# Kernel optimization log

Hardware: AMD Instinct MI355X
Metric: run time of the kernel (lower is better)

Reference implementation:

```python
import jax, jax.numpy as jnp
import numpy as np

NB_CLASSES = 10
NB_NEIGHBORS = 75  # 1 closest + 74 precomputed geodesic neighbors


def setup_inputs() -> dict:
    key = jax.random.key(0)
    k0, k1, k2, k3, k4, k5 = jax.random.split(key, 6)
    nb_data, nb_train, d = 1024, 100000, 256
    x = jax.random.normal(k0, (nb_data, d), dtype=jnp.float32)
    X = jax.random.normal(k1, (nb_train, d), dtype=jnp.float32)
    # train table is stored normalized + centered (init_nn_querier)
    X = X / jnp.linalg.norm(X, axis=1, keepdims=True)
    X = X - jnp.mean(X, axis=0)
    center = jax.random.normal(k2, (d,), dtype=jnp.float32) * 0.01
    train_labels = jax.random.randint(k3, (nb_train,), 0, NB_CLASSES).astype(jnp.int32)
    train_neighbor_index = jax.random.randint(
        k4, (nb_train, NB_NEIGHBORS - 1), 0, nb_train).astype(jnp.int32)
    cali_nonconformity = jnp.sort(
        jax.random.randint(k5, (1000,), 0, NB_NEIGHBORS)).astype(jnp.int32)
    return {
        "x": x, "X": X, "center": center,
        "train_labels": train_labels,
        "train_neighbor_index": train_neighbor_index,
        "cali_nonconformity": cali_nonconformity,
    }


def reference(x, X, center, train_labels, train_neighbor_index, cali_nonconformity):
    # --- find_train_knns: normalize query, center, closest-neighbor search ---
    xq = x / jnp.linalg.norm(x, axis=1, keepdims=True) - center  # [B, d]
    # squared euclidean distances to every train point: [B, nb_train]
    d2 = (jnp.sum(xq * xq, axis=1, keepdims=True)
          - 2.0 * (xq @ X.T)
          + jnp.sum(X * X, axis=1)[None, :])
    closest = jnp.argmin(d2, axis=1)                               # [B]
    # neighbor list = closest point prepended to its precomputed table row
    neigh = jnp.concatenate(
        [closest[:, None], train_neighbor_index[closest]], axis=1)  # [B, K]
    knns_labels = train_labels[neigh]                              # [B, K]
    # --- nonconformity: per-class bincount, #knns NOT in class ---
    counts = jnp.sum(jax.nn.one_hot(knns_labels, NB_CLASSES, dtype=jnp.int32),
                     axis=1)                                       # [B, C]
    knns_not_in_class = jnp.sum(counts, axis=1, keepdims=True) - counts
    # --- preds_conf_cred: conformal p-values via bisect_left ---
    nb_cali = cali_nonconformity.shape[0]
    pos = jnp.searchsorted(cali_nonconformity, knns_not_in_class, side='left')
    p_value = (nb_cali - pos).astype(jnp.float32) / float(nb_cali)  # [B, C]
    preds = jnp.argmax(p_value, axis=1)                             # [B]
    top2, _ = jax.lax.top_k(p_value, 2)                             # [B, 2]
    nb_data = p_value.shape[0]
    creds = jnp.zeros_like(p_value).at[jnp.arange(nb_data), preds].set(top2[:, 0])
    return creds
```

## Files before the change

### kernel.cpp

```cpp
#include <hip/hip_runtime.h>
#include <stdint.h>


typedef __attribute__((ext_vector_type(8))) short short8;
typedef __attribute__((ext_vector_type(4))) float float4v;

static __device__ __forceinline__ unsigned short bf16_rn(float f) {
    unsigned int u = __float_as_uint(f);
    unsigned int r = (u + 0x7FFFu + ((u >> 16) & 1u)) >> 16;
    return (unsigned short)r;
}

static __device__ __forceinline__ void gload_lds16(const void* g, void* l) {
    __builtin_amdgcn_global_load_lds(
        (const __attribute__((address_space(1))) unsigned int*)g,
        (__attribute__((address_space(3))) unsigned int*)l, 16, 0, 0);
}

__global__ __launch_bounds__(256) void prep_all(
    const float* __restrict__ X, const float* __restrict__ x,
    const float* __restrict__ center,
    unsigned short* __restrict__ Bh, float* __restrict__ xn2,
    unsigned short* __restrict__ Ah, float* __restrict__ xqf,
    float* __restrict__ q2a, float* __restrict__ al2q,
    unsigned int* __restrict__ scal,
    int nb_train, int Np, int B, int Mp, int train_rb)
{
    const int tid = threadIdx.x;
    __shared__ float smax[16];
    __shared__ float p1[4], p2[4], p3[4];

    if ((int)blockIdx.x < train_rb) {
        const int r   = blockIdx.x * 16 + (tid >> 4);
        const int seg = tid & 15;
        if (r >= nb_train) {
            ushort4 z = make_ushort4(0, 0, 0, 0);
            ushort4* bp = (ushort4*)(Bh + (size_t)r * 256 + seg * 16);
            bp[0] = z; bp[1] = z; bp[2] = z; bp[3] = z;
            if (seg == 0) { xn2[r] = 3.0e38f; smax[tid >> 4] = 0.f; }
        } else {
            const float* xr = X + (size_t)r * 256 + seg * 16;
            float4 v0 = ((const float4*)xr)[0];
            float4 v1 = ((const float4*)xr)[1];
            float4 v2 = ((const float4*)xr)[2];
            float4 v3 = ((const float4*)xr)[3];
            ushort4 h0, h1, h2, h3;
            h0.x = bf16_rn(v0.x); h0.y = bf16_rn(v0.y); h0.z = bf16_rn(v0.z); h0.w = bf16_rn(v0.w);
            h1.x = bf16_rn(v1.x); h1.y = bf16_rn(v1.y); h1.z = bf16_rn(v1.z); h1.w = bf16_rn(v1.w);
            h2.x = bf16_rn(v2.x); h2.y = bf16_rn(v2.y); h2.z = bf16_rn(v2.z); h2.w = bf16_rn(v2.w);
            h3.x = bf16_rn(v3.x); h3.y = bf16_rn(v3.y); h3.z = bf16_rn(v3.z); h3.w = bf16_rn(v3.w);
            ushort4* bp = (ushort4*)(Bh + (size_t)r * 256 + seg * 16);
            bp[0] = h0; bp[1] = h1; bp[2] = h2; bp[3] = h3;
            float ss = v0.x * v0.x + v0.y * v0.y + v0.z * v0.z + v0.w * v0.w
                     + v1.x * v1.x + v1.y * v1.y + v1.z * v1.z + v1.w * v1.w
                     + v2.x * v2.x + v2.y * v2.y + v2.z * v2.z + v2.w * v2.w
                     + v3.x * v3.x + v3.y * v3.y + v3.z * v3.z + v3.w * v3.w;
            ss += __shfl_xor(ss, 1);
            ss += __shfl_xor(ss, 2);
            ss += __shfl_xor(ss, 4);
            ss += __shfl_xor(ss, 8);
            if (seg == 0) { xn2[r] = ss; smax[tid >> 4] = ss; }
        }
        __syncthreads();
        if (tid == 0) {
            float m = smax[0];
            #pragma unroll
            for (int i = 1; i < 16; ++i) m = fmaxf(m, smax[i]);
            if (m > 0.f) atomicMax(scal, __float_as_uint(m));
        }
        return;
    }
    int row = blockIdx.x - train_rb;
    if (row >= Mp) return;
    if (row >= B) {
        Ah[(size_t)row * 256 + tid] = 0;
        xqf[(size_t)row * 256 + tid] = 0.f;
        if (tid == 0) { q2a[row] = 0.f; al2q[row] = 0.f; }
        return;
    }
    float v = x[(size_t)row * 256 + tid];
    float ss = v * v;
    #pragma unroll
    for (int s = 1; s < 64; s <<= 1) ss += __shfl_xor(ss, s);
    if ((tid & 63) == 0) p1[tid >> 6] = ss;
    __syncthreads();
    float tot = p1[0] + p1[1] + p1[2] + p1[3];
    float inv = 1.0f / sqrtf(tot);
    float val = v * inv - center[tid];
    unsigned short hb = bf16_rn(val);
    float hf = __uint_as_float((unsigned int)hb << 16);
    float al = val - hf;
    Ah[(size_t)row * 256 + tid] = hb;
    xqf[(size_t)row * 256 + tid] = val;
    float ss2 = val * val, sal = al * al;
    #pragma unroll
    for (int s = 1; s < 64; s <<= 1) {
        ss2 += __shfl_xor(ss2, s);
        sal += __shfl_xor(sal, s);
    }
    if ((tid & 63) == 0) { p2[tid >> 6] = ss2; p3[tid >> 6] = sal; }
    __syncthreads();
    if (tid == 0) {
        q2a[row]  = p2[0] + p2[1] + p2[2] + p2[3];
        al2q[row] = p3[0] + p3[1] + p3[2] + p3[3];
    }
}

__global__ __launch_bounds__(256, 4) void mfma_tile(
    const unsigned short* __restrict__ Adata,
    const unsigned short* __restrict__ Bdata,
    const float* __restrict__ xn2,
    float* __restrict__ gmin,
    int Mp, int Np, int nb_train, int B,
    int ntiles, int nper, int mtiles)
{
    __shared__ unsigned short As[128 * 64];
    __shared__ unsigned short Bs[128 * 64];

    const int bid = blockIdx.x;
    const int xcd = bid & 7;
    const int s_  = bid >> 3;
    const int n_t = xcd * nper + (s_ / mtiles);
    const int m_t = s_ - (s_ / mtiles) * mtiles;
    if (n_t >= ntiles) return;
    const int mtile = m_t * 128;
    const int ntile = n_t * 128;

    const int tid  = threadIdx.x;
    const int wave = tid >> 6;
    const int lane = tid & 63;

    const int isB   = wave >> 1;
    const int Rwave = (wave & 1) * 64;
    const int lrow8  = lane >> 3;
    const int lchunk = lane & 7;
    const unsigned short* sbase = isB
        ? (Bdata + (size_t)(ntile + Rwave + lrow8) * 256 + (size_t)((lchunk ^ lrow8) * 8))
        : (Adata + (size_t)(mtile + Rwave + lrow8) * 256 + (size_t)((lchunk ^ lrow8) * 8));
    unsigned short* lwave = (isB ? Bs : As) + Rwave * 64;

    const int mq = (wave >> 1) * 64;
    const int nq = (wave & 1) * 64;
    const int lrow = lane & 15;
    const int kseg = lane >> 4;
    const int sw = lrow & 7;

    float4v acc[4][4];
    #pragma unroll
    for (int i = 0; i < 4; ++i)
        #pragma unroll
        for (int j = 0; j < 4; ++j)
            acc[i][j] = (float4v){0.f, 0.f, 0.f, 0.f};

    for (int s = 0; s < 4; ++s) {
        const unsigned short* g = sbase + (size_t)(s * 64);
        __syncthreads();
        #pragma unroll
        for (int q = 0; q < 8; ++q)
            gload_lds16(g + q * 2048, lwave + q * 512);
        __syncthreads();
        #pragma unroll
        for (int t = 0; t < 2; ++t) {
            const int wch = ((t * 4 + kseg) ^ sw) * 8;
            short8 a[4], b[4];
            #pragma unroll
            for (int i = 0; i < 4; ++i)
                a[i] = *(const short8*)&As[(mq + i * 16 + lrow) * 64 + wch];
            #pragma unroll
            for (int j = 0; j < 4; ++j)
                b[j] = *(const short8*)&Bs[(nq + j * 16 + lrow) * 64 + wch];
            #pragma unroll
            for (int i = 0; i < 4; ++i)
                #pragma unroll
                for (int j = 0; j < 4; ++j)
                    acc[i][j] = __builtin_amdgcn_mfma_f32_16x16x32_bf16(
                        a[i], b[j], acc[i][j], 0, 0, 0);
        }
    }

    const int ng64 = Np >> 6;
    const int gb = (ntile + nq) >> 6;
    float xnv[4];
    #pragma unroll
    for (int j = 0; j < 4; ++j)
        xnv[j] = xn2[ntile + nq + j * 16 + lrow];

    #pragma unroll
    for (int i = 0; i < 4; ++i) {
        #pragma unroll
        for (int r = 0; r < 4; ++r) {
            const int lm = mq + i * 16 + kseg * 4 + r;
            const int gq = mtile + lm;
            float vm = fminf(
                fminf(xnv[0] - 2.0f * acc[i][0][r], xnv[1] - 2.0f * acc[i][1][r]),
                fminf(xnv[2] - 2.0f * acc[i][2][r], xnv[3] - 2.0f * acc[i][3][r]));
            #pragma unroll
            for (int sft = 1; sft < 16; sft <<= 1)
                vm = fminf(vm, __shfl_xor(vm, sft));
            if (lrow == 0 && gq < B)
                gmin[(size_t)gq * ng64 + gb] = vm;
        }
    }
}

__global__ __launch_bounds__(256) void select_classify(
    const float* __restrict__ gmin, const float* __restrict__ xqf,
    const float* __restrict__ X, const float* __restrict__ xn2,
    const float* __restrict__ q2a, const float* __restrict__ al2q,
    const unsigned int* __restrict__ scal,
    const int* __restrict__ labels, const int* __restrict__ nbr,
    const int* __restrict__ cali, float* __restrict__ out,
    int Np, int nb_train, int knm1, int nb_cali, int B)
{
    extern __shared__ float gbuf[];
    __shared__ float xq_s[256];
    __shared__ float wmin[4], fsc[4];
    __shared__ int   fid[4];
    __shared__ float s_thr;
    __shared__ int   cand[256];
    __shared__ int   s_ncand;
    __shared__ int   s_closest;

    const int q    = blockIdx.x;
    const int tid  = threadIdx.x;
    const int lane = tid & 63;
    const int wave = tid >> 6;
    const int ng64 = Np >> 6;

    if (tid == 0) s_ncand = 0;
    xq_s[tid] = xqf[(size_t)q * 256 + tid];
    float vmin = 3.4e38f;
    for (int i = tid; i < ng64; i += 256) {
        float v = gmin[(size_t)q * ng64 + i];
        gbuf[i] = v;
        vmin = fminf(vmin, v);
    }
    #pragma unroll
    for (int s = 1; s < 64; s <<= 1) vmin = fminf(vmin, __shfl_xor(vmin, s));
    if (lane == 0) wmin[wave] = vmin;
    __syncthreads();
    if (tid == 0) {
        float m = fminf(fminf(wmin[0], wmin[1]), fminf(wmin[2], wmin[3]));
        float maxb  = sqrtf(__uint_as_float(scal[0]));
        float maxbl = maxb * 0.00390625f;
        float an = sqrtf(q2a[q]), al = sqrtf(al2q[q]);
        float errdot = al * maxb * 1.00390625f + (an + al) * maxbl;
        s_thr = m + 4.0f * errdot + 1e-3f;
    }
    __syncthreads();
    const float thr = s_thr;
    for (int g = tid; g < ng64; g += 256) {
        if (gbuf[g] <= thr) {
            int p = atomicAdd(&s_ncand, 1);
            if (p < 256) cand[p] = g;
        }
    }
    __syncthreads();
    const int nc = s_ncand;

    const int rsub = tid & 3;
    const int rrow = tid >> 2;
    float bsc = 3.4e38f; int bidx = 0x7FFFFFFF;
    auto rescore = [&](int g) {
        int row = g * 64 + rrow;
        if (row < nb_train) {
            const float* xr = X + (size_t)row * 256 + rsub * 64;
            const float* xs = xq_s + rsub * 64;
            float dot = 0.f;
            #pragma unroll
            for (int k = 0; k < 16; ++k) {
                float4 a4 = *(const float4*)(xs + k * 4);
                float4 b4 = *(const float4*)(xr + k * 4);
                dot += a4.x * b4.x + a4.y * b4.y + a4.z * b4.z + a4.w * b4.w;
            }
            dot += __shfl_xor(dot, 1);
            dot += __shfl_xor(dot, 2);
            float sc = xn2[row] - 2.0f * dot;
            if (sc < bsc || (sc == bsc && row < bidx)) { bsc = sc; bidx = row; }
        }
    };
    if (nc <= 256) {
        for (int c = 0; c < nc; ++c) rescore(cand[c]);
    } else {
        for (int g = 0; g < ng64; ++g)
            if (gbuf[g] <= thr) rescore(g);
    }
    #pragma unroll
    for (int s = 1; s < 64; s <<= 1) {
        float osc = __shfl_xor(bsc, s);
        int   oid = __shfl_xor(bidx, s);
        if (osc < bsc || (osc == bsc && oid < bidx)) { bsc = osc; bidx = oid; }
    }
    if (lane == 0) { fsc[wave] = bsc; fid[wave] = bidx; }
    __syncthreads();
    if (tid == 0) {
        float bs = fsc[0]; int bi = fid[0];
        #pragma unroll
        for (int w = 1; w < 4; ++w)
            if (fsc[w] < bs || (fsc[w] == bs && fid[w] < bi)) { bs = fsc[w]; bi = fid[w]; }
        s_closest = bi;
    }
    __syncthreads();

    if (wave == 0) {
        const int closest = s_closest;
        const int K = knm1 + 1;
        int lbl0 = -1, lbl1 = -1;
        if (lane < K) {
            int idx = (lane == 0) ? closest : nbr[(size_t)closest * knm1 + (lane - 1)];
            lbl0 = labels[idx];
        }
        int j2 = lane + 64;
        if (j2 < K) {
            int idx = nbr[(size_t)closest * knm1 + (j2 - 1)];
            lbl1 = labels[idx];
        }
        int bestc = 0, bestp = -1;
        #pragma unroll
        for (int c = 0; c < 10; ++c) {
            int cnt = __popcll(__ballot(lbl0 == c)) + __popcll(__ballot(lbl1 == c));
            int v = K - cnt;
            int lo = 0, hi = nb_cali;
            while (lo < hi) {
                int mid = (lo + hi) >> 1;
                if (cali[mid] < v) lo = mid + 1; else hi = mid;
            }
            int p = nb_cali - lo;
            if (p > bestp) { bestp = p; bestc = c; }
        }
        float pv = (float)bestp / (float)nb_cali;
        if (lane < 10)
            out[(size_t)q * 10 + lane] = (lane == bestc) ? pv : 0.0f;
    }
}

extern "C" void kernel_launch(void* const* d_in, const int* in_sizes, int n_in,
                              void* d_out, int out_size, void* d_ws, size_t ws_size,
                              hipStream_t stream) {
    const float* x      = (const float*)d_in[0];
    const float* X      = (const float*)d_in[1];
    const float* center = (const float*)d_in[2];
    const int* labels   = (const int*)d_in[3];
    const int* nbr      = (const int*)d_in[4];
    const int* cali     = (const int*)d_in[5];
    float* out = (float*)d_out;

    const int d        = in_sizes[2];
    const int B        = in_sizes[0] / d;
    const int nb_train = in_sizes[3];
    const int knm1     = in_sizes[4] / nb_train;
    const int nb_cali  = in_sizes[5];

    const int Mp = (B + 127) & ~127;
    const int Np = (nb_train + 127) & ~127;
    const int ng64 = Np >> 6;

    char* ws = (char*)d_ws;
    size_t off = 0;
    float* gmin = (float*)(ws + off);          off += (size_t)Mp * ng64 * 4;
    unsigned short* Ah = (unsigned short*)(ws + off); off += (size_t)Mp * 256 * 2;
    float* xqf  = (float*)(ws + off);          off += (size_t)Mp * 256 * 4;
    float* q2a  = (float*)(ws + off);          off += (size_t)Mp * 4;
    float* al2q = (float*)(ws + off);          off += (size_t)Mp * 4;
    unsigned short* Bh = (unsigned short*)(ws + off); off += (size_t)Np * 256 * 2;
    float* xn2  = (float*)(ws + off);          off += (size_t)Np * 4;
    unsigned int* scal = (unsigned int*)(ws + off); off += 8;

    hipMemsetAsync(scal, 0, 8, stream);

    const int train_rb = Np / 16;
    prep_all<<<train_rb + Mp, 256, 0, stream>>>(
        X, x, center, Bh, xn2, Ah, xqf, q2a, al2q, scal,
        nb_train, Np, B, Mp, train_rb);

    const int ntiles = Np / 128;
    const int mtiles = Mp / 128;
    const int nper   = (ntiles + 7) / 8;
    mfma_tile<<<8 * nper * mtiles, 256, 0, stream>>>(
        Ah, Bh, xn2, gmin, Mp, Np, nb_train, B, ntiles, nper, mtiles);

    select_classify<<<B, 256, ng64 * 4, stream>>>(
        gmin, xqf, X, xn2, q2a, al2q, scal, labels, nbr, cali, out,
        Np, nb_train, knm1, nb_cali, B);
}
```

Before: 339.7 us.

## Fuse train-table bf16 conversion into GEMM tile kernel with resident B tile

Drops the separate pass that converts the train table to bf16 in global memory. Each workgroup now loads its own 128-row train tile from fp32, converts it into LDS, and keeps it resident while streaming four query tiles through double-buffered LDS staging. This is meant to remove the round trip of writing and re-reading the bf16 train table, and to reuse each B tile across several query tiles. In exchange the train tile is converted twice (once per query half) and LDS use grows to about 96KB, which limits occupancy to one workgroup per CU.

```diff
diff --git a/kernel.cpp b/kernel.cpp
--- a/kernel.cpp
+++ b/kernel.cpp
@@ -17,60 +17,14 @@
         (__attribute__((address_space(3))) unsigned int*)l, 16, 0, 0);
 }
 
-__global__ __launch_bounds__(256) void prep_all(
-    const float* __restrict__ X, const float* __restrict__ x,
-    const float* __restrict__ center,
-    unsigned short* __restrict__ Bh, float* __restrict__ xn2,
+__global__ __launch_bounds__(256) void prep_q(
+    const float* __restrict__ x, const float* __restrict__ center,
     unsigned short* __restrict__ Ah, float* __restrict__ xqf,
-    float* __restrict__ q2a, float* __restrict__ al2q,
-    unsigned int* __restrict__ scal,
-    int nb_train, int Np, int B, int Mp, int train_rb)
+    float* __restrict__ q2a, float* __restrict__ al2q, int B, int Mp)
 {
     const int tid = threadIdx.x;
-    __shared__ float smax[16];
+    const int row = blockIdx.x;
     __shared__ float p1[4], p2[4], p3[4];
-
-    if ((int)blockIdx.x < train_rb) {
-        const int r   = blockIdx.x * 16 + (tid >> 4);
-        const int seg = tid & 15;
-        if (r >= nb_train) {
-            ushort4 z = make_ushort4(0, 0, 0, 0);
-            ushort4* bp = (ushort4*)(Bh + (size_t)r * 256 + seg * 16);
-            bp[0] = z; bp[1] = z; bp[2] = z; bp[3] = z;
-            if (seg == 0) { xn2[r] = 3.0e38f; smax[tid >> 4] = 0.f; }
-        } else {
-            const float* xr = X + (size_t)r * 256 + seg * 16;
-            float4 v0 = ((const float4*)xr)[0];
-            float4 v1 = ((const float4*)xr)[1];
-            float4 v2 = ((const float4*)xr)[2];
-            float4 v3 = ((const float4*)xr)[3];
-            ushort4 h0, h1, h2, h3;
-            h0.x = bf16_rn(v0.x); h0.y = bf16_rn(v0.y); h0.z = bf16_rn(v0.z); h0.w = bf16_rn(v0.w);
-            h1.x = bf16_rn(v1.x); h1.y = bf16_rn(v1.y); h1.z = bf16_rn(v1.z); h1.w = bf16_rn(v1.w);
-            h2.x = bf16_rn(v2.x); h2.y = bf16_rn(v2.y); h2.z = bf16_rn(v2.z); h2.w = bf16_rn(v2.w);
-            h3.x = bf16_rn(v3.x); h3.y = bf16_rn(v3.y); h3.z = bf16_rn(v3.z); h3.w = bf16_rn(v3.w);
-            ushort4* bp = (ushort4*)(Bh + (size_t)r * 256 + seg * 16);
-            bp[0] = h0; bp[1] = h1; bp[2] = h2; bp[3] = h3;
-            float ss = v0.x * v0.x + v0.y * v0.y + v0.z * v0.z + v0.w * v0.w
-                     + v1.x * v1.x + v1.y * v1.y + v1.z * v1.z + v1.w * v1.w
-                     + v2.x * v2.x + v2.y * v2.y + v2.z * v2.z + v2.w * v2.w
-                     + v3.x * v3.x + v3.y * v3.y + v3.z * v3.z + v3.w * v3.w;
-            ss += __shfl_xor(ss, 1);
-            ss += __shfl_xor(ss, 2);
-            ss += __shfl_xor(ss, 4);
-            ss += __shfl_xor(ss, 8);
-            if (seg == 0) { xn2[r] = ss; smax[tid >> 4] = ss; }
-        }
-        __syncthreads();
-        if (tid == 0) {
-            float m = smax[0];
-            #pragma unroll
-            for (int i = 1; i < 16; ++i) m = fmaxf(m, smax[i]);
-            if (m > 0.f) atomicMax(scal, __float_as_uint(m));
-        }
-        return;
-    }
-    int row = blockIdx.x - train_rb;
     if (row >= Mp) return;
     if (row >= B) {
         Ah[(size_t)row * 256 + tid] = 0;
@@ -106,44 +60,102 @@
     }
 }
 
-__global__ __launch_bounds__(256, 4) void mfma_tile(
-    const unsigned short* __restrict__ Adata,
-    const unsigned short* __restrict__ Bdata,
-    const float* __restrict__ xn2,
-    float* __restrict__ gmin,
-    int Mp, int Np, int nb_train, int B,
-    int ntiles, int nper, int mtiles)
+__global__ __launch_bounds__(256, 1) void fused_tile(
+    const float* __restrict__ X, const unsigned short* __restrict__ Ah,
+    float* __restrict__ xn2, float* __restrict__ gmin,
+    unsigned int* __restrict__ scal,
+    int Mp, int Np, int nb_train, int B, int ntiles)
 {
-    __shared__ unsigned short As[128 * 64];
-    __shared__ unsigned short Bs[128 * 64];
-
-    const int bid = blockIdx.x;
-    const int xcd = bid & 7;
-    const int s_  = bid >> 3;
-    const int n_t = xcd * nper + (s_ / mtiles);
-    const int m_t = s_ - (s_ / mtiles) * mtiles;
-    if (n_t >= ntiles) return;
-    const int mtile = m_t * 128;
-    const int ntile = n_t * 128;
+    __shared__ unsigned short Bsf[4 * 128 * 64];
+    __shared__ unsigned short As[2][128 * 64];
+    __shared__ float xnl[128];
+    __shared__ float mx4[4];
+
+    const int nwg  = ntiles * 2;
+    const int orig = blockIdx.x;
+    const int xcd  = orig & 7;
+    const int pos  = orig >> 3;
+    const int q8   = nwg >> 3, r8 = nwg & 7;
+    const int wg   = (xcd < r8 ? xcd * (q8 + 1) : r8 * (q8 + 1) + (xcd - r8) * q8) + pos;
+    if (wg >= nwg) return;
+    const int nt = wg >> 1, mh = wg & 1;
+    const int ntile = nt * 128;
 
     const int tid  = threadIdx.x;
     const int wave = tid >> 6;
     const int lane = tid & 63;
 
-    const int isB   = wave >> 1;
-    const int Rwave = (wave & 1) * 64;
-    const int lrow8  = lane >> 3;
-    const int lchunk = lane & 7;
-    const unsigned short* sbase = isB
-        ? (Bdata + (size_t)(ntile + Rwave + lrow8) * 256 + (size_t)((lchunk ^ lrow8) * 8))
-        : (Adata + (size_t)(mtile + Rwave + lrow8) * 256 + (size_t)((lchunk ^ lrow8) * 8));
-    unsigned short* lwave = (isB ? Bs : As) + Rwave * 64;
+    {
+        const int r = tid >> 1, h = tid & 1;
+        const int grow = ntile + r;
+        const bool pad = (grow >= nb_train);
+        float ss = 0.f;
+        if (!pad) {
+            const float4* src = (const float4*)(X + (size_t)grow * 256 + h * 128);
+            #pragma unroll
+            for (int g2 = 0; g2 < 8; ++g2) {
+                float4 f0 = src[g2 * 4 + 0], f1 = src[g2 * 4 + 1];
+                float4 f2 = src[g2 * 4 + 2], f3 = src[g2 * 4 + 3];
+                short8 c0, c1;
+                c0[0] = bf16_rn(f0.x); c0[1] = bf16_rn(f0.y);
+                c0[2] = bf16_rn(f0.z); c0[3] = bf16_rn(f0.w);
+                c0[4] = bf16_rn(f1.x); c0[5] = bf16_rn(f1.y);
+                c0[6] = bf16_rn(f1.z); c0[7] = bf16_rn(f1.w);
+                c1[0] = bf16_rn(f2.x); c1[1] = bf16_rn(f2.y);
+                c1[2] = bf16_rn(f2.z); c1[3] = bf16_rn(f2.w);
+                c1[4] = bf16_rn(f3.x); c1[5] = bf16_rn(f3.y);
+                c1[6] = bf16_rn(f3.z); c1[7] = bf16_rn(f3.w);
+                const int C0 = h * 16 + g2 * 2, C1 = C0 + 1;
+                *(short8*)&Bsf[(C0 >> 3) * 8192 + r * 64 + ((C0 & 7) ^ (r & 7)) * 8] = c0;
+                *(short8*)&Bsf[(C1 >> 3) * 8192 + r * 64 + ((C1 & 7) ^ (r & 7)) * 8] = c1;
+                ss += f0.x * f0.x + f0.y * f0.y + f0.z * f0.z + f0.w * f0.w
+                    + f1.x * f1.x + f1.y * f1.y + f1.z * f1.z + f1.w * f1.w
+                    + f2.x * f2.x + f2.y * f2.y + f2.z * f2.z + f2.w * f2.w
+                    + f3.x * f3.x + f3.y * f3.y + f3.z * f3.z + f3.w * f3.w;
+            }
+        } else {
+            short8 z = {0, 0, 0, 0, 0, 0, 0, 0};
+            #pragma unroll
+            for (int g2 = 0; g2 < 8; ++g2) {
+                const int C0 = h * 16 + g2 * 2, C1 = C0 + 1;
+                *(short8*)&Bsf[(C0 >> 3) * 8192 + r * 64 + ((C0 & 7) ^ (r & 7)) * 8] = z;
+                *(short8*)&Bsf[(C1 >> 3) * 8192 + r * 64 + ((C1 & 7) ^ (r & 7)) * 8] = z;
+            }
+        }
+        float tot = ss + __shfl_xor(ss, 1);
+        float xv  = pad ? 3.0e38f : tot;
+        if (h == 0) {
+            xnl[r] = xv;
+            if (mh == 0) xn2[grow] = xv;
+        }
+        float c = (h == 0 && !pad) ? tot : 0.f;
+        #pragma unroll
+        for (int s = 1; s < 64; s <<= 1) c = fmaxf(c, __shfl_xor(c, s));
+        if (lane == 0) mx4[wave] = c;
+    }
 
     const int mq = (wave >> 1) * 64;
     const int nq = (wave & 1) * 64;
     const int lrow = lane & 15;
     const int kseg = lane >> 4;
     const int sw = lrow & 7;
+    const int srow = lane >> 3;
+    const int schk = ((lane & 7) ^ (lane >> 3)) * 8;
+    const int ng64 = Np >> 6;
+    const int gb   = (ntile + nq) >> 6;
+
+    auto stageA = [&](int s) {
+        const int mt2 = s >> 2, ks2 = s & 3;
+        const int mbase = (mh * 4 + mt2) * 128;
+        unsigned short* dbuf = As[s & 1];
+        #pragma unroll
+        for (int q = 0; q < 4; ++q) {
+            const int s8 = wave * 4 + q;
+            const unsigned short* src =
+                Ah + (size_t)(mbase + s8 * 8 + srow) * 256 + ks2 * 64 + schk;
+            gload_lds16(src, dbuf + s8 * 512);
+        }
+    };
 
     float4v acc[4][4];
     #pragma unroll
@@ -152,23 +164,27 @@
         for (int j = 0; j < 4; ++j)
             acc[i][j] = (float4v){0.f, 0.f, 0.f, 0.f};
 
-    for (int s = 0; s < 4; ++s) {
-        const unsigned short* g = sbase + (size_t)(s * 64);
-        __syncthreads();
-        #pragma unroll
-        for (int q = 0; q < 8; ++q)
-            gload_lds16(g + q * 2048, lwave + q * 512);
-        __syncthreads();
+    stageA(0);
+    __syncthreads();
+    if (tid == 0 && mh == 0) {
+        float m = fmaxf(fmaxf(mx4[0], mx4[1]), fmaxf(mx4[2], mx4[3]));
+        if (m > 0.f) atomicMax(scal, __float_as_uint(m));
+    }
+
+    for (int s = 0; s < 16; ++s) {
+        if (s + 1 < 16) stageA(s + 1);
+        const unsigned short* Ab = As[s & 1];
+        const unsigned short* Bb = &Bsf[(s & 3) * 8192];
         #pragma unroll
         for (int t = 0; t < 2; ++t) {
             const int wch = ((t * 4 + kseg) ^ sw) * 8;
             short8 a[4], b[4];
             #pragma unroll
             for (int i = 0; i < 4; ++i)
-                a[i] = *(const short8*)&As[(mq + i * 16 + lrow) * 64 + wch];
+                a[i] = *(const short8*)&Ab[(mq + i * 16 + lrow) * 64 + wch];
             #pragma unroll
             for (int j = 0; j < 4; ++j)
-                b[j] = *(const short8*)&Bs[(nq + j * 16 + lrow) * 64 + wch];
+                b[j] = *(const short8*)&Bb[(nq + j * 16 + lrow) * 64 + wch];
             #pragma unroll
             for (int i = 0; i < 4; ++i)
                 #pragma unroll
@@ -176,29 +192,35 @@
                     acc[i][j] = __builtin_amdgcn_mfma_f32_16x16x32_bf16(
                         a[i], b[j], acc[i][j], 0, 0, 0);
         }
-    }
-
-    const int ng64 = Np >> 6;
-    const int gb = (ntile + nq) >> 6;
-    float xnv[4];
-    #pragma unroll
-    for (int j = 0; j < 4; ++j)
-        xnv[j] = xn2[ntile + nq + j * 16 + lrow];
-
-    #pragma unroll
-    for (int i = 0; i < 4; ++i) {
-        #pragma unroll
-        for (int r = 0; r < 4; ++r) {
-            const int lm = mq + i * 16 + kseg * 4 + r;
-            const int gq = mtile + lm;
-            float vm = fminf(
-                fminf(xnv[0] - 2.0f * acc[i][0][r], xnv[1] - 2.0f * acc[i][1][r]),
-                fminf(xnv[2] - 2.0f * acc[i][2][r], xnv[3] - 2.0f * acc[i][3][r]));
-            #pragma unroll
-            for (int sft = 1; sft < 16; sft <<= 1)
-                vm = fminf(vm, __shfl_xor(vm, sft));
-            if (lrow == 0 && gq < B)
-                gmin[(size_t)gq * ng64 + gb] = vm;
+        __syncthreads();
+
+        if ((s & 3) == 3) {
+            const int mtile = (mh * 4 + (s >> 2)) * 128;
+            float xnv[4];
+            #pragma unroll
+            for (int j = 0; j < 4; ++j)
+                xnv[j] = xnl[nq + j * 16 + lrow];
+            #pragma unroll
+            for (int i = 0; i < 4; ++i) {
+                #pragma unroll
+                for (int r = 0; r < 4; ++r) {
+                    const int lm = mq + i * 16 + kseg * 4 + r;
+                    const int gq = mtile + lm;
+                    float vm = fminf(
+                        fminf(xnv[0] - 2.0f * acc[i][0][r], xnv[1] - 2.0f * acc[i][1][r]),
+                        fminf(xnv[2] - 2.0f * acc[i][2][r], xnv[3] - 2.0f * acc[i][3][r]));
+                    #pragma unroll
+                    for (int sft = 1; sft < 16; sft <<= 1)
+                        vm = fminf(vm, __shfl_xor(vm, sft));
+                    if (lrow == 0 && gq < B)
+                        gmin[(size_t)gq * ng64 + gb] = vm;
+                }
+            }
+            #pragma unroll
+            for (int i = 0; i < 4; ++i)
+                #pragma unroll
+                for (int j = 0; j < 4; ++j)
+                    acc[i][j] = (float4v){0.f, 0.f, 0.f, 0.f};
         }
     }
 }
@@ -362,22 +384,16 @@
     float* xqf  = (float*)(ws + off);          off += (size_t)Mp * 256 * 4;
     float* q2a  = (float*)(ws + off);          off += (size_t)Mp * 4;
     float* al2q = (float*)(ws + off);          off += (size_t)Mp * 4;
-    unsigned short* Bh = (unsigned short*)(ws + off); off += (size_t)Np * 256 * 2;
     float* xn2  = (float*)(ws + off);          off += (size_t)Np * 4;
     unsigned int* scal = (unsigned int*)(ws + off); off += 8;
 
     hipMemsetAsync(scal, 0, 8, stream);
 
-    const int train_rb = Np / 16;
-    prep_all<<<train_rb + Mp, 256, 0, stream>>>(
-        X, x, center, Bh, xn2, Ah, xqf, q2a, al2q, scal,
-        nb_train, Np, B, Mp, train_rb);
+    prep_q<<<Mp, 256, 0, stream>>>(x, center, Ah, xqf, q2a, al2q, B, Mp);
 
     const int ntiles = Np / 128;
-    const int mtiles = Mp / 128;
-    const int nper   = (ntiles + 7) / 8;
-    mfma_tile<<<8 * nper * mtiles, 256, 0, stream>>>(
-        Ah, Bh, xn2, gmin, Mp, Np, nb_train, B, ntiles, nper, mtiles);
+    fused_tile<<<ntiles * 2, 256, 0, stream>>>(
+        X, Ah, xn2, gmin, scal, Mp, Np, nb_train, B, ntiles);
 
     select_classify<<<B, 256, ng64 * 4, stream>>>(
         gmin, xqf, X, xn2, q2a, al2q, scal, labels, nbr, cali, out,
```

After: 419.0 us. 1.23x slower.
